# Optimization experiments

Hardware: AMD Instinct MI355X
Metric: run time of the kernel (lower is better)

## Reference

```python
import jax, jax.numpy as jnp
import numpy as np

V, D, NL, N, ED, K, DT = 32000, 256, 4, 16, 512, 4, 16  # dt_rank = ceil(256/16)
B, L = 2, 2048
EPS = 1e-5


def setup_inputs() -> dict:
    key = jax.random.key(0)
    ks = jax.random.split(key, 10)
    s = 0.02
    x = jax.random.randint(ks[0], (B, L), 0, V)
    embed_t = jax.random.normal(ks[1], (V, D)) * s
    rms_w = jnp.ones((NL, D))
    in_proj_w = jax.random.normal(ks[2], (NL, 2 * ED, D)) * s
    conv_w = jax.random.normal(ks[3], (NL, ED, K)) * 0.1
    conv_b = jnp.zeros((NL, ED))
    x_proj_w = jax.random.normal(ks[4], (NL, DT + 2 * N, ED)) * s
    dt_proj_w = jax.random.normal(ks[5], (NL, ED, DT)) * (DT ** -0.5)
    dt_proj_b = jax.random.uniform(ks[6], (NL, ED), minval=-4.0, maxval=-2.0)  # softplus -> small dt
    A_log = jnp.log(jnp.tile(jnp.arange(1, N + 1, dtype=jnp.float32), (NL, ED, 1)))  # S4D-real init
    D_p = jnp.ones((NL, ED))
    out_proj_w = jax.random.normal(ks[7], (NL, D, ED)) * s
    norm_w = jnp.ones(D)
    norm_b = jnp.zeros(D)
    head_w = jax.random.normal(ks[8], (V, D)) * s
    head_b = jnp.zeros(V)
    return dict(x=x, embed_t=embed_t, rms_w=rms_w, in_proj_w=in_proj_w, conv_w=conv_w,
                conv_b=conv_b, x_proj_w=x_proj_w, dt_proj_w=dt_proj_w, dt_proj_b=dt_proj_b,
                A_log=A_log, D_p=D_p, out_proj_w=out_proj_w, norm_w=norm_w, norm_b=norm_b,
                head_w=head_w, head_b=head_b)


def _rmsnorm(x, w):
    return x * jax.lax.rsqrt(jnp.mean(x * x, axis=-1, keepdims=True) + EPS) * w


def _layernorm(x, w, b):
    mu = jnp.mean(x, axis=-1, keepdims=True)
    var = jnp.mean((x - mu) ** 2, axis=-1, keepdims=True)
    return (x - mu) * jax.lax.rsqrt(var + EPS) * w + b


def _scan_combine(left, right):
    al, bl = left
    ar, br = right
    return (al * ar, ar * bl + br)


def _mamba_block(h, rw, ipw, cw, cb, xpw, dpw, dpb, alog, dp, opw):
    # h: (B, L, D). Residual block: h + mixer(rmsnorm(h))
    xin = _rmsnorm(h, rw)
    xz = xin @ ipw.T                      # (B, L, 2*ED)
    xc, z = jnp.split(xz, 2, axis=-1)
    # causal depthwise conv1d, kernel K, left-pad K-1 (== torch padding=K-1 then [:L])
    k = cw.shape[1]
    seqlen = xc.shape[1]
    xp = jnp.pad(xc, ((0, 0), (k - 1, 0), (0, 0)))
    xc = sum(xp[:, i:i + seqlen, :] * cw[:, i] for i in range(k)) + cb
    xc = jax.nn.silu(xc)
    # selective SSM
    dt_rank = dpw.shape[1]
    n = alog.shape[1]
    dbc = xc @ xpw.T                      # (B, L, dt_rank + 2N)
    delta, Bm, Cm = jnp.split(dbc, [dt_rank, dt_rank + n], axis=-1)
    delta = jax.nn.softplus(delta @ dpw.T + dpb)   # (B, L, ED)
    A = -jnp.exp(alog)                              # (ED, N)
    dA = jnp.exp(delta[..., None] * A)              # (B, L, ED, N)
    dBx = (delta[..., None] * Bm[:, :, None, :]) * xc[..., None]  # (B, L, ED, N)
    _, hs = jax.lax.associative_scan(_scan_combine, (dA, dBx), axis=1)  # h_t = dA_t*h_{t-1} + dBx_t
    y = jnp.einsum('blen,bln->ble', hs, Cm) + dp * xc
    y = y * jax.nn.silu(z)
    return h + y @ opw.T


def reference(x, embed_t, rms_w, in_proj_w, conv_w, conv_b, x_proj_w, dt_proj_w,
              dt_proj_b, A_log, D_p, out_proj_w, norm_w, norm_b, head_w, head_b):
    h = embed_t[x]                        # (B, L, D)
    for i in range(rms_w.shape[0]):
        h = _mamba_block(h, rms_w[i], in_proj_w[i], conv_w[i], conv_b[i], x_proj_w[i],
                         dt_proj_w[i], dt_proj_b[i], A_log[i], D_p[i], out_proj_w[i])
    hn = _layernorm(h, norm_w, norm_b)
    return hn @ head_w.T + head_b         # (B, L, V)
```

## Files before the change

kernel.cpp:

```cpp
#include <hip/hip_runtime.h>
#include <hip/hip_bf16.h>
#include <math.h>

#define Bq   2
#define Lq   2048
#define Dq   256
#define NLq  4
#define Nst  16
#define EDq  512
#define Kq   4
#define DTq  16
#define Vq   32000
#define Rq   (Bq*Lq)
#define NCq  256
#define LCq  (Lq/NCq)

typedef __attribute__((ext_vector_type(8))) __bf16 bf16x8v;
typedef __attribute__((ext_vector_type(4))) float f32x4v;
typedef __attribute__((address_space(1))) const void GV;
typedef __attribute__((address_space(3))) void LV;

__device__ __forceinline__ unsigned short to_bf16(float f) {
    unsigned int u = __float_as_uint(f);
    unsigned int r = (u + 0x7FFFu + ((u >> 16) & 1u)) >> 16;
    return (unsigned short)r;
}
__device__ __forceinline__ float from_bf16(unsigned short u) {
    return __uint_as_float(((unsigned int)u) << 16);
}

__global__ __launch_bounds__(256) void convert_bf16(const float* __restrict__ in,
                                                    unsigned short* __restrict__ out, int n) {
    int i = (blockIdx.x * 256 + threadIdx.x) * 4;
    if (i + 3 < n) {
        float4 v = *(const float4*)&in[i];
        ushort4 o;
        o.x = to_bf16(v.x); o.y = to_bf16(v.y); o.z = to_bf16(v.z); o.w = to_bf16(v.w);
        *(ushort4*)&out[i] = o;
    }
}

__global__ __launch_bounds__(256) void embed_kernel(const int* __restrict__ x,
                                                    const float* __restrict__ et,
                                                    float* __restrict__ h) {
    int r = blockIdx.x;
    int d = threadIdx.x;
    h[r * Dq + d] = et[x[r] * Dq + d];
}

__global__ __launch_bounds__(256) void rmsnorm_kernel(const float* __restrict__ h,
                                                      const float* __restrict__ w,
                                                      unsigned short* __restrict__ out) {
    int r = blockIdx.x;
    int d = threadIdx.x;
    float v = h[r * Dq + d];
    float ss = v * v;
#pragma unroll
    for (int o = 32; o > 0; o >>= 1) ss += __shfl_down(ss, o);
    __shared__ float sb[4];
    if ((threadIdx.x & 63) == 0) sb[threadIdx.x >> 6] = ss;
    __syncthreads();
    float tot = sb[0] + sb[1] + sb[2] + sb[3];
    float scale = rsqrtf(tot * (1.0f / Dq) + 1e-5f);
    out[r * Dq + d] = to_bf16(v * scale * w[d]);
}

__global__ __launch_bounds__(256) void layernorm_kernel(const float* __restrict__ h,
                                                        const float* __restrict__ w,
                                                        const float* __restrict__ b,
                                                        unsigned short* __restrict__ out) {
    int r = blockIdx.x;
    int d = threadIdx.x;
    float v = h[r * Dq + d];
    float s = v, s2 = v * v;
#pragma unroll
    for (int o = 32; o > 0; o >>= 1) { s += __shfl_down(s, o); s2 += __shfl_down(s2, o); }
    __shared__ float sb[8];
    if ((threadIdx.x & 63) == 0) { sb[threadIdx.x >> 6] = s; sb[4 + (threadIdx.x >> 6)] = s2; }
    __syncthreads();
    float S  = sb[0] + sb[1] + sb[2] + sb[3];
    float S2 = sb[4] + sb[5] + sb[6] + sb[7];
    float mu = S * (1.0f / Dq);
    float var = S2 * (1.0f / Dq) - mu * mu;
    out[r * Dq + d] = to_bf16((v - mu) * rsqrtf(var + 1e-5f) * w[d] + b[d]);
}

template<int BM, int BN, typename OT, bool ACC>
__global__ __launch_bounds__(256) void gemm_mfma(const unsigned short* __restrict__ A,
                                                 const unsigned short* __restrict__ W,
                                                 const float* __restrict__ bias,
                                                 OT* __restrict__ C,
                                                 int M, int N, int K) {
    constexpr int WGM = (BM == 128 && BN == 128) ? 2 : (BM == 128 ? 4 : 2);
    constexpr int WGN = 4 / WGM;
    constexpr int MR = BM / (WGM * 16);
    constexpr int NR = BN / (WGN * 16);
    constexpr int AR = BM / 64;
    constexpr int BR = BN / 64;
    __shared__ unsigned short As[BM * 32];
    __shared__ unsigned short Bs[BN * 32];

    const int gx = gridDim.x;
    const int nwg = gx * gridDim.y;
    int flat = blockIdx.y * gx + blockIdx.x;
    if ((nwg & 7) == 0) {
        int cpx = nwg >> 3;
        flat = (flat & 7) * cpx + (flat >> 3);
    }
    const int m0 = (flat / gx) * BM, n0 = (flat % gx) * BN;

    const int tid = threadIdx.x;
    const int wid = tid >> 6, lane = tid & 63;
    const int wrow = (wid / WGN) * (BM / WGM);
    const int wcol = (wid % WGN) * (BN / WGN);

    f32x4v acc[MR][NR];
#pragma unroll
    for (int i = 0; i < MR; i++)
#pragma unroll
        for (int j = 0; j < NR; j++) acc[i][j] = (f32x4v){0.f, 0.f, 0.f, 0.f};

    const int srow = lane >> 2;
    const int skoff = (lane & 3) * 8;
    const unsigned short* gA = A + (size_t)(m0 + wid * (16 * AR) + srow) * K + skoff;
    unsigned short* lA = As + wid * (512 * AR) + lane * 8;
    const unsigned short* gW = W + (size_t)(n0 + wid * (16 * BR) + srow) * K + skoff;
    unsigned short* lB = Bs + wid * (512 * BR) + lane * 8;

    const int l15 = lane & 15, lk = (lane >> 4) * 8;

    for (int kt = 0; kt < K; kt += 32) {
        __syncthreads();
#pragma unroll
        for (int p = 0; p < AR; p++)
            __builtin_amdgcn_global_load_lds((GV*)(gA + kt + (size_t)p * 16 * K),
                                             (LV*)(lA + p * 512), 16, 0, 0);
#pragma unroll
        for (int p = 0; p < BR; p++)
            __builtin_amdgcn_global_load_lds((GV*)(gW + kt + (size_t)p * 16 * K),
                                             (LV*)(lB + p * 512), 16, 0, 0);
        __syncthreads();

        bf16x8v a[MR], b[NR];
#pragma unroll
        for (int i = 0; i < MR; i++)
            a[i] = *(const bf16x8v*)&As[(wrow + i * 16 + l15) * 32 + lk];
#pragma unroll
        for (int j = 0; j < NR; j++)
            b[j] = *(const bf16x8v*)&Bs[(wcol + j * 16 + l15) * 32 + lk];
#pragma unroll
        for (int i = 0; i < MR; i++)
#pragma unroll
            for (int j = 0; j < NR; j++)
                acc[i][j] = __builtin_amdgcn_mfma_f32_16x16x32_bf16(a[i], b[j], acc[i][j], 0, 0, 0);
    }

    const int rbase = m0 + wrow + (lane >> 4) * 4;
    const int cbase = n0 + wcol + l15;
#pragma unroll
    for (int i = 0; i < MR; i++) {
#pragma unroll
        for (int j = 0; j < NR; j++) {
            int col = cbase + j * 16;
            float bv = bias ? bias[col] : 0.f;
#pragma unroll
            for (int r = 0; r < 4; r++) {
                int row = rbase + i * 16 + r;
                float v = acc[i][j][r] + bv;
                OT* dst = &C[(size_t)row * N + col];
                if constexpr (ACC) { *dst = v + *dst; }
                else if constexpr (__is_same(OT, unsigned short)) { *dst = to_bf16(v); }
                else { *dst = v; }
            }
        }
    }
}

__global__ __launch_bounds__(256) void mid_fused(const unsigned short* __restrict__ xz,
                                                 const float* __restrict__ cw,
                                                 const float* __restrict__ cb,
                                                 const unsigned short* __restrict__ xpw16,
                                                 const float* __restrict__ dtw,
                                                 const float* __restrict__ dtb,
                                                 unsigned short* __restrict__ xc,
                                                 float* __restrict__ dbc,
                                                 float* __restrict__ dlt) {
    const int r = blockIdx.x;
    const int l = r & (Lq - 1);
    const int tid = threadIdx.x;
    __shared__ float xcs[EDq];
    __shared__ float dbs[16];

#pragma unroll
    for (int p = 0; p < 2; p++) {
        int e = tid + p * 256;
        float acc = cb[e];
#pragma unroll
        for (int i = 0; i < 4; i++) {
            int dl = i - 3;
            if (l + dl >= 0)
                acc = fmaf(from_bf16(xz[(size_t)(r + dl) * 1024 + e]), cw[e * 4 + i], acc);
        }
        float s = acc / (1.0f + __expf(-acc));
        xcs[e] = s;
        xc[(size_t)r * EDq + e] = to_bf16(s);
    }
    __syncthreads();

    const int j = tid >> 2, sub = tid & 3;
    float part = 0.f;
    if (j < 48) {
        const unsigned short* wr = &xpw16[j * EDq + sub * 128];
        const float* xr = &xcs[sub * 128];
        for (int k = 0; k < 128; k += 4) {
            ushort4 wv = *(const ushort4*)&wr[k];
            float4 xv = *(const float4*)&xr[k];
            part = fmaf(from_bf16(wv.x), xv.x, part);
            part = fmaf(from_bf16(wv.y), xv.y, part);
            part = fmaf(from_bf16(wv.z), xv.z, part);
            part = fmaf(from_bf16(wv.w), xv.w, part);
        }
    }
    part += __shfl_xor(part, 1);
    part += __shfl_xor(part, 2);
    if (j < 48 && sub == 0) {
        dbc[(size_t)r * 48 + j] = part;
        if (j < 16) dbs[j] = part;
    }
    __syncthreads();

#pragma unroll
    for (int p = 0; p < 2; p++) {
        int e = tid + p * 256;
        const float* wr = &dtw[e * 16];
        float acc = dtb[e];
#pragma unroll
        for (int k = 0; k < 16; k++) acc = fmaf(dbs[k], wr[k], acc);
        float sp = (acc > 20.f) ? acc : log1pf(__expf(acc));
        dlt[(size_t)r * EDq + e] = sp;
    }
}

__global__ __launch_bounds__(256) void scan_pass1(const float* __restrict__ dlt,
                                                  const unsigned short* __restrict__ xc,
                                                  const float* __restrict__ dbc,
                                                  const float* __restrict__ A_log,
                                                  float* __restrict__ cA,
                                                  float* __restrict__ cB) {
    int gid = blockIdx.x * 256 + threadIdx.x;
    int e = gid & (EDq - 1);
    int bc = gid >> 9;
    int rbase = bc * LCq;

    float Aa[16];
#pragma unroll
    for (int n = 0; n < 16; n++) Aa[n] = -__expf(A_log[e * 16 + n]);
    float pA[16], hB[16];
#pragma unroll
    for (int n = 0; n < 16; n++) { pA[n] = 1.f; hB[n] = 0.f; }

    for (int t = 0; t < LCq; t++) {
        int r = rbase + t;
        float d = dlt[(size_t)r * EDq + e];
        float xv = from_bf16(xc[(size_t)r * EDq + e]);
        float dx = d * xv;
        const float4* Bp = (const float4*)&dbc[(size_t)r * 48 + 16];
        float4 B0 = Bp[0], B1 = Bp[1], B2 = Bp[2], B3 = Bp[3];
        float Bm[16] = {B0.x, B0.y, B0.z, B0.w, B1.x, B1.y, B1.z, B1.w,
                        B2.x, B2.y, B2.z, B2.w, B3.x, B3.y, B3.z, B3.w};
#pragma unroll
        for (int n = 0; n < 16; n++) {
            float dA = __expf(d * Aa[n]);
            hB[n] = fmaf(dA, hB[n], dx * Bm[n]);
            pA[n] *= dA;
        }
    }
    size_t ob = (size_t)gid * 16;
#pragma unroll
    for (int n = 0; n < 16; n++) { cA[ob + n] = pA[n]; cB[ob + n] = hB[n]; }
}

__global__ __launch_bounds__(64) void scan_combine(const float* __restrict__ cA,
                                                   const float* __restrict__ cB,
                                                   float* __restrict__ cP) {
    int idx = blockIdx.x * 64 + threadIdx.x;
    int en = idx & 8191;
    int b = idx >> 13;
    float hc = 0.f;
    for (int c = 0; c < NCq; c++) {
        size_t base = ((size_t)(b * NCq + c) << 13) + en;
        cP[base] = hc;
        hc = fmaf(cA[base], hc, cB[base]);
    }
}

__global__ __launch_bounds__(256) void scan_pass2(const float* __restrict__ dlt,
                                                  const unsigned short* __restrict__ xc,
                                                  const float* __restrict__ dbc,
                                                  const float* __restrict__ A_log,
                                                  const float* __restrict__ cP,
                                                  const float* __restrict__ Dp,
                                                  const unsigned short* __restrict__ xz,
                                                  unsigned short* __restrict__ y) {
    int gid = blockIdx.x * 256 + threadIdx.x;
    int e = gid & (EDq - 1);
    int bc = gid >> 9;
    int rbase = bc * LCq;

    float Aa[16];
#pragma unroll
    for (int n = 0; n < 16; n++) Aa[n] = -__expf(A_log[e * 16 + n]);
    float hh[16];
    size_t pb = (size_t)gid * 16;
#pragma unroll
    for (int n = 0; n < 16; n++) hh[n] = cP[pb + n];
    float Dv = Dp[e];

    for (int t = 0; t < LCq; t++) {
        int r = rbase + t;
        float d = dlt[(size_t)r * EDq + e];
        float xv = from_bf16(xc[(size_t)r * EDq + e]);
        float dx = d * xv;
        const float4* Bp = (const float4*)&dbc[(size_t)r * 48 + 16];
        float4 B0 = Bp[0], B1 = Bp[1], B2 = Bp[2], B3 = Bp[3];
        float Bm[16] = {B0.x, B0.y, B0.z, B0.w, B1.x, B1.y, B1.z, B1.w,
                        B2.x, B2.y, B2.z, B2.w, B3.x, B3.y, B3.z, B3.w};
        const float4* Cp = (const float4*)&dbc[(size_t)r * 48 + 32];
        float4 C0 = Cp[0], C1 = Cp[1], C2 = Cp[2], C3 = Cp[3];
        float Cm[16] = {C0.x, C0.y, C0.z, C0.w, C1.x, C1.y, C1.z, C1.w,
                        C2.x, C2.y, C2.z, C2.w, C3.x, C3.y, C3.z, C3.w};
        float cacc = 0.f;
#pragma unroll
        for (int n = 0; n < 16; n++) {
            float dA = __expf(d * Aa[n]);
            hh[n] = fmaf(dA, hh[n], dx * Bm[n]);
            cacc = fmaf(hh[n], Cm[n], cacc);
        }
        float yv = fmaf(Dv, xv, cacc);
        float zv = from_bf16(xz[(size_t)r * 1024 + EDq + e]);
        float sz = zv / (1.0f + __expf(-zv));
        y[(size_t)r * EDq + e] = to_bf16(yv * sz);
    }
}

extern "C" void kernel_launch(void* const* d_in, const int* in_sizes, int n_in,
                              void* d_out, int out_size, void* d_ws, size_t ws_size,
                              hipStream_t stream) {
    const int*   x         = (const int*)d_in[0];
    const float* embed_t   = (const float*)d_in[1];
    const float* rms_w     = (const float*)d_in[2];
    const float* in_proj_w = (const float*)d_in[3];
    const float* conv_w    = (const float*)d_in[4];
    const float* conv_b    = (const float*)d_in[5];
    const float* x_proj_w  = (const float*)d_in[6];
    const float* dt_proj_w = (const float*)d_in[7];
    const float* dt_proj_b = (const float*)d_in[8];
    const float* A_log     = (const float*)d_in[9];
    const float* D_p       = (const float*)d_in[10];
    const float* out_proj_w= (const float*)d_in[11];
    const float* norm_w    = (const float*)d_in[12];
    const float* norm_b    = (const float*)d_in[13];
    const float* head_w    = (const float*)d_in[14];
    const float* head_b    = (const float*)d_in[15];
    float* out = (float*)d_out;

    const size_t CSZ = (size_t)Bq * NCq * EDq * Nst;

    float* ws = (float*)d_ws;
    float* h    = ws;
    float* dbc  = h   + (size_t)Rq * Dq;
    float* dlt  = dbc + (size_t)Rq * 48;
    float* cA   = dlt + (size_t)Rq * EDq;
    float* cB   = cA  + CSZ;
    float* cP   = cB  + CSZ;
    float* fend = cP  + CSZ;

    unsigned short* xz16  = (unsigned short*)fend;
    unsigned short* xc16  = xz16  + (size_t)Rq * 1024;
    unsigned short* xin16 = xc16  + (size_t)Rq * EDq;
    unsigned short* yb16  = xin16 + (size_t)Rq * Dq;
    unsigned short* hn16  = yb16  + (size_t)Rq * EDq;
    unsigned short* w16i  = hn16  + (size_t)Rq * Dq;
    unsigned short* w16o  = w16i  + (size_t)NLq * 1024 * Dq;
    unsigned short* w16xp = w16o  + (size_t)NLq * Dq * EDq;
    unsigned short* w16h  = w16xp + (size_t)NLq * 48 * EDq;

    convert_bf16<<<(NLq * 1024 * Dq) / 1024, 256, 0, stream>>>(in_proj_w, w16i, NLq * 1024 * Dq);
    convert_bf16<<<(NLq * Dq * EDq) / 1024, 256, 0, stream>>>(out_proj_w, w16o, NLq * Dq * EDq);
    convert_bf16<<<(NLq * 48 * EDq) / 1024, 256, 0, stream>>>(x_proj_w, w16xp, NLq * 48 * EDq);
    convert_bf16<<<(Vq * Dq) / 1024, 256, 0, stream>>>(head_w, w16h, Vq * Dq);

    embed_kernel<<<Rq, 256, 0, stream>>>(x, embed_t, h);

    for (int i = 0; i < NLq; i++) {
        rmsnorm_kernel<<<Rq, 256, 0, stream>>>(h, rms_w + i * Dq, xin16);
        gemm_mfma<128, 64, unsigned short, false><<<dim3(1024 / 64, Rq / 128), 256, 0, stream>>>(
            xin16, w16i + (size_t)i * 1024 * Dq, nullptr, xz16, Rq, 1024, Dq);
        mid_fused<<<Rq, 256, 0, stream>>>(
            xz16, conv_w + i * EDq * Kq, conv_b + i * EDq,
            w16xp + (size_t)i * 48 * EDq,
            dt_proj_w + (size_t)i * EDq * DTq, dt_proj_b + i * EDq,
            xc16, dbc, dlt);
        scan_pass1<<<(Bq * NCq * EDq) / 256, 256, 0, stream>>>(
            dlt, xc16, dbc, A_log + i * EDq * Nst, cA, cB);
        scan_combine<<<(Bq * EDq * Nst) / 64, 64, 0, stream>>>(cA, cB, cP);
        scan_pass2<<<(Bq * NCq * EDq) / 256, 256, 0, stream>>>(
            dlt, xc16, dbc, A_log + i * EDq * Nst, cP, D_p + i * EDq, xz16, yb16);
        gemm_mfma<64, 64, float, true><<<dim3(Dq / 64, Rq / 64), 256, 0, stream>>>(
            yb16, w16o + (size_t)i * Dq * EDq, nullptr, h, Rq, Dq, EDq);
    }

    layernorm_kernel<<<Rq, 256, 0, stream>>>(h, norm_w, norm_b, hn16);
    gemm_mfma<128, 128, float, false><<<dim3(Vq / 128, Rq / 128), 256, 0, stream>>>(
        hn16, w16h, head_b, out, Rq, Vq, Dq);
}
```

Before: 699.3 us.

## Split SSM state dimension across 4 lanes and use fewer longer scan chunks

The chunked selective scan now assigns each (chunk, channel) to four threads, each owning 4 of the 16 state entries. The C-projection is reduced across the four lanes with xor shuffles. The chunk count drops from 256 to 64 (32 steps per chunk), and the combine kernel switches to 256-thread blocks. This shrinks the cA/cB/cP traffic and the serial combine length, and cuts per-thread registers so occupancy can rise. In exchange, each thread loops serially over 4x more steps, the per-step delta/x loads are duplicated across the four lanes, and only one lane in four does the output epilogue.

```diff
diff --git a/kernel.cpp b/kernel.cpp
--- a/kernel.cpp
+++ b/kernel.cpp
@@ -12,8 +12,8 @@
 #define DTq  16
 #define Vq   32000
 #define Rq   (Bq*Lq)
-#define NCq  256
-#define LCq  (Lq/NCq)
+#define NCv  64
+#define LCv  (Lq/NCv)
 
 typedef __attribute__((ext_vector_type(8))) __bf16 bf16x8v;
 typedef __attribute__((ext_vector_type(4))) float f32x4v;
@@ -248,47 +248,45 @@
                                                   float* __restrict__ cA,
                                                   float* __restrict__ cB) {
     int gid = blockIdx.x * 256 + threadIdx.x;
-    int e = gid & (EDq - 1);
-    int bc = gid >> 9;
-    int rbase = bc * LCq;
-
-    float Aa[16];
-#pragma unroll
-    for (int n = 0; n < 16; n++) Aa[n] = -__expf(A_log[e * 16 + n]);
-    float pA[16], hB[16];
-#pragma unroll
-    for (int n = 0; n < 16; n++) { pA[n] = 1.f; hB[n] = 0.f; }
-
-    for (int t = 0; t < LCq; t++) {
+    int sub = gid & 3;
+    int e = (gid >> 2) & (EDq - 1);
+    int bc = gid >> 11;
+    int rbase = bc * LCv;
+
+    float Aa[4];
+#pragma unroll
+    for (int k = 0; k < 4; k++) Aa[k] = -__expf(A_log[e * 16 + sub * 4 + k]);
+    float pA[4] = {1.f, 1.f, 1.f, 1.f};
+    float hB[4] = {0.f, 0.f, 0.f, 0.f};
+
+    for (int t = 0; t < LCv; t++) {
         int r = rbase + t;
         float d = dlt[(size_t)r * EDq + e];
         float xv = from_bf16(xc[(size_t)r * EDq + e]);
         float dx = d * xv;
-        const float4* Bp = (const float4*)&dbc[(size_t)r * 48 + 16];
-        float4 B0 = Bp[0], B1 = Bp[1], B2 = Bp[2], B3 = Bp[3];
-        float Bm[16] = {B0.x, B0.y, B0.z, B0.w, B1.x, B1.y, B1.z, B1.w,
-                        B2.x, B2.y, B2.z, B2.w, B3.x, B3.y, B3.z, B3.w};
-#pragma unroll
-        for (int n = 0; n < 16; n++) {
-            float dA = __expf(d * Aa[n]);
-            hB[n] = fmaf(dA, hB[n], dx * Bm[n]);
-            pA[n] *= dA;
-        }
-    }
-    size_t ob = (size_t)gid * 16;
-#pragma unroll
-    for (int n = 0; n < 16; n++) { cA[ob + n] = pA[n]; cB[ob + n] = hB[n]; }
-}
-
-__global__ __launch_bounds__(64) void scan_combine(const float* __restrict__ cA,
-                                                   const float* __restrict__ cB,
-                                                   float* __restrict__ cP) {
-    int idx = blockIdx.x * 64 + threadIdx.x;
+        float4 Bm = *(const float4*)&dbc[(size_t)r * 48 + 16 + sub * 4];
+        float Bk[4] = {Bm.x, Bm.y, Bm.z, Bm.w};
+#pragma unroll
+        for (int k = 0; k < 4; k++) {
+            float dA = __expf(d * Aa[k]);
+            hB[k] = fmaf(dA, hB[k], dx * Bk[k]);
+            pA[k] *= dA;
+        }
+    }
+    size_t ob = ((size_t)bc * EDq + e) * 16 + sub * 4;
+    *(float4*)&cA[ob] = make_float4(pA[0], pA[1], pA[2], pA[3]);
+    *(float4*)&cB[ob] = make_float4(hB[0], hB[1], hB[2], hB[3]);
+}
+
+__global__ __launch_bounds__(256) void scan_combine(const float* __restrict__ cA,
+                                                    const float* __restrict__ cB,
+                                                    float* __restrict__ cP) {
+    int idx = blockIdx.x * 256 + threadIdx.x;
     int en = idx & 8191;
     int b = idx >> 13;
     float hc = 0.f;
-    for (int c = 0; c < NCq; c++) {
-        size_t base = ((size_t)(b * NCq + c) << 13) + en;
+    for (int c = 0; c < NCv; c++) {
+        size_t base = ((size_t)(b * NCv + c) << 13) + en;
         cP[base] = hc;
         hc = fmaf(cA[base], hc, cB[base]);
     }
@@ -303,43 +301,46 @@
                                                   const unsigned short* __restrict__ xz,
                                                   unsigned short* __restrict__ y) {
     int gid = blockIdx.x * 256 + threadIdx.x;
-    int e = gid & (EDq - 1);
-    int bc = gid >> 9;
-    int rbase = bc * LCq;
-
-    float Aa[16];
-#pragma unroll
-    for (int n = 0; n < 16; n++) Aa[n] = -__expf(A_log[e * 16 + n]);
-    float hh[16];
-    size_t pb = (size_t)gid * 16;
-#pragma unroll
-    for (int n = 0; n < 16; n++) hh[n] = cP[pb + n];
-    float Dv = Dp[e];
-
-    for (int t = 0; t < LCq; t++) {
+    int sub = gid & 3;
+    int e = (gid >> 2) & (EDq - 1);
+    int bc = gid >> 11;
+    int rbase = bc * LCv;
+
+    float Aa[4];
+#pragma unroll
+    for (int k = 0; k < 4; k++) Aa[k] = -__expf(A_log[e * 16 + sub * 4 + k]);
+    float hh[4];
+    size_t pb = ((size_t)bc * EDq + e) * 16 + sub * 4;
+    {
+        float4 v = *(const float4*)&cP[pb];
+        hh[0] = v.x; hh[1] = v.y; hh[2] = v.z; hh[3] = v.w;
+    }
+    const float Dv = Dp[e];
+
+    for (int t = 0; t < LCv; t++) {
         int r = rbase + t;
         float d = dlt[(size_t)r * EDq + e];
         float xv = from_bf16(xc[(size_t)r * EDq + e]);
         float dx = d * xv;
-        const float4* Bp = (const float4*)&dbc[(size_t)r * 48 + 16];
-        float4 B0 = Bp[0], B1 = Bp[1], B2 = Bp[2], B3 = Bp[3];
-        float Bm[16] = {B0.x, B0.y, B0.z, B0.w, B1.x, B1.y, B1.z, B1.w,
-                        B2.x, B2.y, B2.z, B2.w, B3.x, B3.y, B3.z, B3.w};
-        const float4* Cp = (const float4*)&dbc[(size_t)r * 48 + 32];
-        float4 C0 = Cp[0], C1 = Cp[1], C2 = Cp[2], C3 = Cp[3];
-        float Cm[16] = {C0.x, C0.y, C0.z, C0.w, C1.x, C1.y, C1.z, C1.w,
-                        C2.x, C2.y, C2.z, C2.w, C3.x, C3.y, C3.z, C3.w};
+        float4 Bm = *(const float4*)&dbc[(size_t)r * 48 + 16 + sub * 4];
+        float4 Cm = *(const float4*)&dbc[(size_t)r * 48 + 32 + sub * 4];
+        float Bk[4] = {Bm.x, Bm.y, Bm.z, Bm.w};
+        float Ck[4] = {Cm.x, Cm.y, Cm.z, Cm.w};
         float cacc = 0.f;
 #pragma unroll
-        for (int n = 0; n < 16; n++) {
-            float dA = __expf(d * Aa[n]);
-            hh[n] = fmaf(dA, hh[n], dx * Bm[n]);
-            cacc = fmaf(hh[n], Cm[n], cacc);
-        }
-        float yv = fmaf(Dv, xv, cacc);
-        float zv = from_bf16(xz[(size_t)r * 1024 + EDq + e]);
-        float sz = zv / (1.0f + __expf(-zv));
-        y[(size_t)r * EDq + e] = to_bf16(yv * sz);
+        for (int k = 0; k < 4; k++) {
+            float dA = __expf(d * Aa[k]);
+            hh[k] = fmaf(dA, hh[k], dx * Bk[k]);
+            cacc = fmaf(hh[k], Ck[k], cacc);
+        }
+        cacc += __shfl_xor(cacc, 1);
+        cacc += __shfl_xor(cacc, 2);
+        if (sub == 0) {
+            float yv = fmaf(Dv, xv, cacc);
+            float zv = from_bf16(xz[(size_t)r * 1024 + EDq + e]);
+            float sz = zv / (1.0f + __expf(-zv));
+            y[(size_t)r * EDq + e] = to_bf16(yv * sz);
+        }
     }
 }
 
@@ -364,7 +365,7 @@
     const float* head_b    = (const float*)d_in[15];
     float* out = (float*)d_out;
 
-    const size_t CSZ = (size_t)Bq * NCq * EDq * Nst;
+    const size_t CSZ = (size_t)Bq * NCv * EDq * Nst;
 
     float* ws = (float*)d_ws;
     float* h    = ws;
@@ -401,10 +402,10 @@
             w16xp + (size_t)i * 48 * EDq,
             dt_proj_w + (size_t)i * EDq * DTq, dt_proj_b + i * EDq,
             xc16, dbc, dlt);
-        scan_pass1<<<(Bq * NCq * EDq) / 256, 256, 0, stream>>>(
+        scan_pass1<<<(Bq * NCv * EDq * 4) / 256, 256, 0, stream>>>(
             dlt, xc16, dbc, A_log + i * EDq * Nst, cA, cB);
-        scan_combine<<<(Bq * EDq * Nst) / 64, 64, 0, stream>>>(cA, cB, cP);
-        scan_pass2<<<(Bq * NCq * EDq) / 256, 256, 0, stream>>>(
+        scan_combine<<<(Bq * EDq * Nst) / 256, 256, 0, stream>>>(cA, cB, cP);
+        scan_pass2<<<(Bq * NCv * EDq * 4) / 256, 256, 0, stream>>>(
             dlt, xc16, dbc, A_log + i * EDq * Nst, cP, D_p + i * EDq, xz16, yb16);
         gemm_mfma<64, 64, float, true><<<dim3(Dq / 64, Rq / 64), 256, 0, stream>>>(
             yb16, w16o + (size_t)i * Dq * EDq, nullptr, h, Rq, Dq, EDq);
```

Result: faster. 664.0 us (-5.0%).
